# Kernel tuning notes

Hardware: AMD Instinct MI355X
Metric: run time of the kernel (lower is better)

Reference implementation:

```python
import jax, jax.numpy as jnp
import numpy as np

B, T, D_IN, D_H, D_CODE, N_CODES, D_OUT = 64, 512, 1024, 512, 256, 128, 100


def setup_inputs() -> dict:
    key = jax.random.key(0)
    ks = jax.random.split(key, 8)
    x = jax.random.normal(ks[0], (B, T, D_IN), dtype=jnp.float32)
    W1 = jax.random.normal(ks[1], (D_IN, D_H), dtype=jnp.float32) * (1.0 / np.sqrt(D_IN))
    b1 = jnp.zeros((D_H,), jnp.float32)
    W2 = jax.random.normal(ks[2], (D_H, D_CODE), dtype=jnp.float32) * (1.0 / np.sqrt(D_H))
    b2 = jnp.zeros((D_CODE,), jnp.float32)
    codebook = jax.random.normal(ks[3], (N_CODES, D_CODE), dtype=jnp.float32)
    Wd = jax.random.normal(ks[4], (D_CODE, D_OUT), dtype=jnp.float32) * (1.0 / np.sqrt(D_CODE))
    bd = jnp.zeros((D_OUT,), jnp.float32)
    return {"x": x, "W1": W1, "b1": b1, "W2": W2, "b2": b2,
            "codebook": codebook, "Wd": Wd, "bd": bd}


def reference(x, W1, b1, W2, b2, codebook, Wd, bd):
    Bb, Tt, _ = x.shape
    # Encoder (per-timestep loop in torch == one batched matmul)
    h = jax.nn.relu(jnp.einsum('btd,dh->bth', x, W1) + b1)
    encoded = jnp.einsum('bth,hc->btc', h, W2) + b2          # [B,T,256]
    flat = encoded.reshape(-1, D_CODE)                        # [B*T,256]
    # Squared euclidean distances (argmin identical to cdist argmin)
    d2 = (jnp.sum(flat * flat, axis=1, keepdims=True)
          - 2.0 * flat @ codebook.T
          + jnp.sum(codebook * codebook, axis=1))             # [B*T,128]
    token_indices = jnp.argmin(d2, axis=-1)                   # [B*T]
    quantized = codebook[token_indices].reshape(Bb, Tt, D_CODE)
    commitment_loss = jnp.mean((encoded - jax.lax.stop_gradient(quantized)) ** 2)
    codebook_loss = jnp.mean((quantized - jax.lax.stop_gradient(encoded)) ** 2)
    # decoded is computed in the torch model but never returned (dead code)
    pooled = encoded.mean(axis=1)
    decoded = pooled @ Wd + bd  # noqa: F841 (pruned by XLA, kept for fidelity)
    total_loss = commitment_loss + 0.25 * codebook_loss
    return (token_indices.reshape(Bb, Tt), commitment_loss, codebook_loss, total_loss)
```

## Files before the change

### kernel.cpp

```cpp
#include <hip/hip_runtime.h>
#include <cstddef>
#include <cstdint>

static constexpr int M_ROWS  = 32768;
static constexpr int D_INK   = 1024;
static constexpr int D_HID   = 512;
static constexpr int D_CODE_ = 256;
static constexpr int N_CODES_= 128;

static constexpr float TAU_GAP = 0.15f;

using f16x8 = __attribute__((ext_vector_type(8))) _Float16;
using f32x4 = __attribute__((ext_vector_type(4))) float;

__device__ __forceinline__ float rdlane(float v, int kk) {
    return __uint_as_float(__builtin_amdgcn_readlane(__float_as_uint(v), kk));
}


__device__ __forceinline__ void dma16(const void* g, void* l) {
    __builtin_amdgcn_global_load_lds(
        (const __attribute__((address_space(1))) void*)g,
        (__attribute__((address_space(3))) void*)l, 16, 0, 0);
}

__device__ __forceinline__ void stage_panel(const _Float16* __restrict__ p,
                                            _Float16* dst, int w, int lane)
{
    #pragma unroll
    for (int ii = 0; ii < 2; ++ii) {
        const int I = 2 * w + ii;
        dma16(p + (size_t)I * 512 + lane * 8, dst + (size_t)I * 512);
    }
}

__device__ __forceinline__ void mfma_tile(const _Float16* sA, const _Float16* sB,
                                          int wm, int wn, int kq, int lm,
                                          f32x4 (&acc)[4][4])
{
    f16x8 a[4];
    #pragma unroll
    for (int fm = 0; fm < 4; ++fm)
        a[fm] = *(const f16x8*)(sA + (kq * 128 + wm * 64 + fm * 16 + lm) * 8);
    #pragma unroll
    for (int fn = 0; fn < 4; ++fn) {
        const f16x8 b = *(const f16x8*)(sB + (kq * 128 + wn * 64 + fn * 16 + lm) * 8);
        #pragma unroll
        for (int fm = 0; fm < 4; ++fm)
            acc[fm][fn] = __builtin_amdgcn_mfma_f32_16x16x32_f16(a[fm], b, acc[fm][fn], 0, 0, 0);
    }
}

__device__ __forceinline__ int xcd_swz(int bid, int nwg) {
    const int q = nwg >> 3;
    return (bid & 7) * q + (bid >> 3);
}

__global__ __launch_bounds__(256)
void prep_cb_kernel(const float* __restrict__ cb, _Float16* __restrict__ cbP,
                    float* __restrict__ cbT,
                    float* __restrict__ cbnorm, float* __restrict__ accum,
                    int* __restrict__ cnt)
{
    const int j = blockIdx.x;
    const int t = threadIdx.x;
    const float v = cb[j * D_CODE_ + t];
    const int ks = t >> 5, kq = (t >> 3) & 3, jj = t & 7;
    cbP[((size_t)ks * 512 + kq * 128 + j) * 8 + jj] = (_Float16)v;
    cbT[(size_t)t * N_CODES_ + j] = v;

    __shared__ float sr[256];
    sr[t] = v * v;
    __syncthreads();
    for (int s = 128; s >= 1; s >>= 1) {
        if (t < s) sr[t] += sr[t + s];
        __syncthreads();
    }
    if (t == 0) cbnorm[j] = sr[0];
    if (j == 0 && t < 2) accum[t] = 0.0f;
    if (j == 0 && t == 2) *cnt = 0;
}

__global__ __launch_bounds__(256)
void pack_w_kernel(const float* __restrict__ W, _Float16* __restrict__ WP,
                   int Kd, int Nd)
{
    const int ks = blockIdx.x, nt = blockIdx.y;
    const int t = threadIdx.x;
    _Float16* dst = WP + ((size_t)nt * (Kd >> 5) + ks) * 4096;
    #pragma unroll
    for (int half = 0; half < 2; ++half) {
        const int f = half * 256 + t;
        const int nc = f & 127, kq = f >> 7;
        f16x8 v;
        #pragma unroll
        for (int j = 0; j < 8; ++j)
            v[j] = (_Float16)W[(size_t)(ks * 32 + kq * 8 + j) * Nd + nt * 128 + nc];
        *(f16x8*)(dst + (size_t)f * 8) = v;
    }
}

__global__ __launch_bounds__(256)
void pack_x_kernel(const float* __restrict__ X, _Float16* __restrict__ XP)
{
    __shared__ _Float16 sh[128][136];
    const int t  = threadIdx.x;
    const int mt = blockIdx.x;
    const int kc = blockIdx.y;

    const float* src = X + (size_t)mt * 128 * D_INK + kc * 128;
    #pragma unroll
    for (int i = 0; i < 16; ++i) {
        const int idx = i * 256 + t;
        const int row = idx >> 5, c4 = idx & 31;
        const float4 v = *(const float4*)(src + (size_t)row * D_INK + c4 * 4);
        _Float16* d = &sh[row][c4 * 4];
        d[0] = (_Float16)v.x; d[1] = (_Float16)v.y;
        d[2] = (_Float16)v.z; d[3] = (_Float16)v.w;
    }
    __syncthreads();

    _Float16* dst = XP + ((size_t)mt * 32 + kc * 4) * 4096;
    #pragma unroll
    for (int s = 0; s < 4; ++s) {
        #pragma unroll
        for (int half = 0; half < 2; ++half) {
            const int f = half * 256 + t;
            const int rc = f & 127, kq = f >> 7;
            const f16x8 v = *(const f16x8*)(&sh[rc][s * 32 + kq * 8]);
            *(f16x8*)(dst + (size_t)s * 4096 + (size_t)f * 8) = v;
        }
    }
}

__global__ __launch_bounds__(256, 4)
void gemm1_kernel(const _Float16* __restrict__ AP, const _Float16* __restrict__ BP,
                  const float* __restrict__ bias, _Float16* __restrict__ CP)
{
    __shared__ _Float16 lds[2][2][4096];

    const int tid  = threadIdx.x;
    const int lane = tid & 63;
    const int w    = tid >> 6;
    const int wm = w >> 1, wn = w & 1;
    const int kq = lane >> 4, lm = lane & 15;

    const int swz = xcd_swz(blockIdx.x, (M_ROWS / 128) * (D_HID / 128));
    const int n0 = (swz & 3) * 128;
    const int m0 = (swz >> 2) * 128;

    const _Float16* Apan = AP + ((size_t)(m0 >> 7) * 32) * 4096;
    const _Float16* Bpan = BP + ((size_t)(n0 >> 7) * 32) * 4096;

    f32x4 acc[4][4] = {};

    stage_panel(Apan, &lds[0][0][0], w, lane);
    stage_panel(Bpan, &lds[0][1][0], w, lane);

    constexpr int NSTEP = D_INK / 32;
    for (int t = 0; t < NSTEP; ++t) {
        const int cur = t & 1, nxt = cur ^ 1;
        __syncthreads();
        if (t + 1 < NSTEP) {
            stage_panel(Apan + (size_t)(t + 1) * 4096, &lds[nxt][0][0], w, lane);
            stage_panel(Bpan + (size_t)(t + 1) * 4096, &lds[nxt][1][0], w, lane);
        }
        mfma_tile(&lds[cur][0][0], &lds[cur][1][0], wm, wn, kq, lm, acc);
    }

    #pragma unroll
    for (int fn = 0; fn < 4; ++fn) {
        const int col = n0 + wn * 64 + fn * 16 + lm;
        const float bv = bias[col];
        #pragma unroll
        for (int fm = 0; fm < 4; ++fm) {
            #pragma unroll
            for (int r = 0; r < 4; ++r) {
                const int row = m0 + wm * 64 + fm * 16 + kq * 4 + r;
                const float v = fmaxf(acc[fm][fn][r] + bv, 0.0f);
                CP[(((size_t)(row >> 7) * 16 + (col >> 5)) * 512
                    + (size_t)((col >> 3) & 3) * 128 + (row & 127)) * 8 + (col & 7)]
                    = (_Float16)v;
            }
        }
    }
}

__global__ __launch_bounds__(256, 4)
void gemm2_kernel(const _Float16* __restrict__ AP, const _Float16* __restrict__ BP,
                  const float* __restrict__ bias, _Float16* __restrict__ CP,
                  float* __restrict__ accum)
{
    __shared__ _Float16 lds[2][2][4096];

    const int tid  = threadIdx.x;
    const int lane = tid & 63;
    const int w    = tid >> 6;
    const int wm = w >> 1, wn = w & 1;
    const int kq = lane >> 4, lm = lane & 15;

    const int swz = xcd_swz(blockIdx.x, (M_ROWS / 128) * (D_CODE_ / 128));
    const int n0 = (swz & 1) * 128;
    const int m0 = (swz >> 1) * 128;

    const _Float16* Apan = AP + ((size_t)(m0 >> 7) * 16) * 4096;
    const _Float16* Bpan = BP + ((size_t)(n0 >> 7) * 16) * 4096;

    f32x4 acc[4][4] = {};

    stage_panel(Apan, &lds[0][0][0], w, lane);
    stage_panel(Bpan, &lds[0][1][0], w, lane);

    constexpr int NSTEP = D_HID / 32;
    for (int t = 0; t < NSTEP; ++t) {
        const int cur = t & 1, nxt = cur ^ 1;
        __syncthreads();
        if (t + 1 < NSTEP) {
            stage_panel(Apan + (size_t)(t + 1) * 4096, &lds[nxt][0][0], w, lane);
            stage_panel(Bpan + (size_t)(t + 1) * 4096, &lds[nxt][1][0], w, lane);
        }
        mfma_tile(&lds[cur][0][0], &lds[cur][1][0], wm, wn, kq, lm, acc);
    }

    float sumsq = 0.0f;
    #pragma unroll
    for (int fn = 0; fn < 4; ++fn) {
        const int col = n0 + wn * 64 + fn * 16 + lm;
        const float bv = bias[col];
        #pragma unroll
        for (int fm = 0; fm < 4; ++fm) {
            #pragma unroll
            for (int r = 0; r < 4; ++r) {
                const int row = m0 + wm * 64 + fm * 16 + kq * 4 + r;
                const float v = acc[fm][fn][r] + bv;
                sumsq = fmaf(v, v, sumsq);
                CP[(((size_t)(row >> 7) * 8 + (col >> 5)) * 512
                    + (size_t)((col >> 3) & 3) * 128 + (row & 127)) * 8 + (col & 7)]
                    = (_Float16)v;
            }
        }
    }
    #pragma unroll
    for (int mk = 1; mk <= 32; mk <<= 1) sumsq += __shfl_xor(sumsq, mk);
    if (lane == 0) atomicAdd(&accum[1], sumsq);
}

__global__ __launch_bounds__(256, 4)
void dist_kernel(const _Float16* __restrict__ AP, const _Float16* __restrict__ BP,
                 const float* __restrict__ cbn,
                 float* __restrict__ outIdx, float* __restrict__ accum,
                 int* __restrict__ cnt, int* __restrict__ list)
{
    __shared__ _Float16 lds[2][2][4096];

    const int tid  = threadIdx.x;
    const int lane = tid & 63;
    const int w    = tid >> 6;
    const int wm = w >> 1, wn = w & 1;
    const int kq = lane >> 4, lm = lane & 15;
    const int m0 = blockIdx.x * 128;

    float cbn_l[4];
    #pragma unroll
    for (int fn = 0; fn < 4; ++fn) cbn_l[fn] = cbn[wn * 64 + fn * 16 + lm];

    const _Float16* Apan = AP + ((size_t)(m0 >> 7) * 8) * 4096;

    f32x4 acc[4][4] = {};

    stage_panel(Apan, &lds[0][0][0], w, lane);
    stage_panel(BP,   &lds[0][1][0], w, lane);

    constexpr int NSTEP = D_CODE_ / 32;
    for (int t = 0; t < NSTEP; ++t) {
        const int cur = t & 1, nxt = cur ^ 1;
        __syncthreads();
        if (t + 1 < NSTEP) {
            stage_panel(Apan + (size_t)(t + 1) * 4096, &lds[nxt][0][0], w, lane);
            stage_panel(BP   + (size_t)(t + 1) * 4096, &lds[nxt][1][0], w, lane);
        }
        mfma_tile(&lds[cur][0][0], &lds[cur][1][0], wm, wn, kq, lm, acc);
    }

    __syncthreads();
    float* eb1 = (float*)&lds[0][0][0];
    float* eb2 = eb1 + 256;
    int*   eix = (int*)(eb2 + 256);

    #pragma unroll
    for (int fm = 0; fm < 4; ++fm) {
        #pragma unroll
        for (int r = 0; r < 4; ++r) {
            float b1v = 3.4e38f, b2v = 3.4e38f; int bi = 0;
            #pragma unroll
            for (int fn = 0; fn < 4; ++fn) {
                const float v = fmaf(-2.0f, acc[fm][fn][r], cbn_l[fn]);
                if (v < b1v) { b2v = b1v; b1v = v; bi = wn * 64 + fn * 16 + lm; }
                else if (v < b2v) b2v = v;
            }
            #pragma unroll
            for (int mk = 1; mk <= 8; mk <<= 1) {
                const float o1 = __shfl_xor(b1v, mk);
                const float o2 = __shfl_xor(b2v, mk);
                const int   oi = __shfl_xor(bi,  mk);
                if (o1 < b1v || (o1 == b1v && oi < bi)) { b2v = fminf(b1v, o2); b1v = o1; bi = oi; }
                else b2v = fminf(b2v, o1);
            }
            const int rl = wm * 64 + fm * 16 + kq * 4 + r;
            if (lm == 0) { eb1[wn * 128 + rl] = b1v; eb2[wn * 128 + rl] = b2v; eix[wn * 128 + rl] = bi; }
        }
    }
    __syncthreads();

    if (tid < 128) {
        const int rl = tid;
        const float a1 = eb1[rl], a2 = eb2[rl]; const int ai = eix[rl];
        const float o1 = eb1[128 + rl], o2 = eb2[128 + rl]; const int oi = eix[128 + rl];
        float B1, B2; int BI;
        if (o1 < a1 || (o1 == a1 && oi < ai)) { B1 = o1; BI = oi; B2 = fminf(a1, o2); }
        else                                  { B1 = a1; BI = ai; B2 = fminf(a2, o1); }
        outIdx[m0 + rl] = (float)BI;
        if (B2 - B1 < TAU_GAP) { const int p = atomicAdd(cnt, 1); list[p] = m0 + rl; }
        float s = B1;
        #pragma unroll
        for (int mk = 1; mk <= 32; mk <<= 1) s += __shfl_xor(s, mk);
        if (lane == 0) atomicAdd(&accum[0], s);
    }
}

__global__ __launch_bounds__(512)
void fixup_kernel(const float* __restrict__ x, const float* __restrict__ W1,
                  const float* __restrict__ b1, const float* __restrict__ W2,
                  const float* __restrict__ b2, const float* __restrict__ cbT,
                  const float* __restrict__ cbnorm,
                  const int* __restrict__ cnt, const int* __restrict__ list,
                  float* __restrict__ outIdx)
{
    __shared__ float xr[8][1024];
    __shared__ float hr[8][512];
    __shared__ float er[8][256];
    __shared__ float dv[8][128];
    __shared__ int   di[8][128];

    const int tid  = threadIdx.x;
    const int lane = tid & 63;
    const int n = *cnt;
    const int ngroups = (n + 7) >> 3;

    for (int g = blockIdx.x; g < ngroups; g += gridDim.x) {
        const int base = g * 8;
        const int nr = n - base < 8 ? n - base : 8;
        __syncthreads();
        #pragma unroll
        for (int r = 0; r < 8; ++r) {
            if (r < nr) {
                const int row = list[base + r];
                *(float2*)&xr[r][tid * 2] =
                    *(const float2*)(x + (size_t)row * D_INK + tid * 2);
            }
        }
        __syncthreads();

        {
            const int c = tid;
            float a[8];
            #pragma unroll
            for (int r = 0; r < 8; ++r) a[r] = 0.f;
            for (int k0 = 0; k0 < D_INK; k0 += 64) {
                float xreg[8];
                #pragma unroll
                for (int r = 0; r < 8; ++r) xreg[r] = xr[r][k0 + lane];
                #pragma unroll 8
                for (int kk = 0; kk < 64; ++kk) {
                    const float wv = W1[(size_t)(k0 + kk) * D_HID + c];
                    #pragma unroll
                    for (int r = 0; r < 8; ++r)
                        a[r] = fmaf(rdlane(xreg[r], kk), wv, a[r]);
                }
            }
            #pragma unroll
            for (int r = 0; r < 8; ++r)
                hr[r][c] = fmaxf(a[r] + b1[c], 0.f);
        }
        __syncthreads();

        {
            const int c = tid & 255, half = tid >> 8;
            float a[4];
            #pragma unroll
            for (int q = 0; q < 4; ++q) a[q] = 0.f;
            for (int k0 = 0; k0 < D_HID; k0 += 64) {
                float hreg[4];
                #pragma unroll
                for (int q = 0; q < 4; ++q) hreg[q] = hr[half * 4 + q][k0 + lane];
                #pragma unroll 8
                for (int kk = 0; kk < 64; ++kk) {
                    const float wv = W2[(size_t)(k0 + kk) * D_CODE_ + c];
                    #pragma unroll
                    for (int q = 0; q < 4; ++q)
                        a[q] = fmaf(rdlane(hreg[q], kk), wv, a[q]);
                }
            }
            #pragma unroll
            for (int q = 0; q < 4; ++q)
                er[half * 4 + q][c] = a[q] + b2[c];
        }
        __syncthreads();

        {
            const int j = tid & 127, rr = tid >> 7;
            float e2[2], dt[2];
            #pragma unroll
            for (int q = 0; q < 2; ++q) { e2[q] = 0.f; dt[q] = 0.f; }
            for (int k0 = 0; k0 < D_CODE_; k0 += 64) {
                float ereg[2];
                ereg[0] = er[rr][k0 + lane];
                ereg[1] = er[rr + 4][k0 + lane];
                #pragma unroll 8
                for (int kk = 0; kk < 64; ++kk) {
                    const float cv = cbT[(size_t)(k0 + kk) * N_CODES_ + j];
                    #pragma unroll
                    for (int q = 0; q < 2; ++q) {
                        const float ev = rdlane(ereg[q], kk);
                        e2[q] = fmaf(ev, ev, e2[q]);
                        dt[q] = fmaf(ev, cv, dt[q]);
                    }
                }
            }
            dv[rr][j]     = (e2[0] - 2.0f * dt[0]) + cbnorm[j];
            di[rr][j]     = j;
            dv[rr + 4][j] = (e2[1] - 2.0f * dt[1]) + cbnorm[j];
            di[rr + 4][j] = j;
        }
        __syncthreads();

        #pragma unroll
        for (int pass = 0; pass < 2; ++pass) {
            const int r = pass * 4 + (tid >> 7);
            const int i = tid & 127;
            for (int st = 64; st >= 1; st >>= 1) {
                if (i < st) {
                    const float a = dv[r][i], b = dv[r][i + st];
                    const int  ib = di[r][i + st];
                    if (b < a || (b == a && ib < di[r][i])) { dv[r][i] = b; di[r][i] = ib; }
                }
                __syncthreads();
            }
        }
        if (tid < nr) outIdx[list[base + tid]] = (float)di[tid][0];
    }
}

__global__ void finalize_kernel(const float* __restrict__ accum, float* __restrict__ out)
{
    const float inv = 1.0f / (32768.0f * 256.0f);
    const float loss = (accum[0] + accum[1]) * inv;
    out[32768] = loss;
    out[32769] = loss;
    out[32770] = 1.25f * loss;
}

extern "C" void kernel_launch(void* const* d_in, const int* in_sizes, int n_in,
                              void* d_out, int out_size, void* d_ws, size_t ws_size,
                              hipStream_t stream)
{
    (void)in_sizes; (void)n_in; (void)out_size; (void)ws_size;

    const float* x  = (const float*)d_in[0];
    const float* W1 = (const float*)d_in[1];
    const float* b1 = (const float*)d_in[2];
    const float* W2 = (const float*)d_in[3];
    const float* b2 = (const float*)d_in[4];
    const float* cb = (const float*)d_in[5];
    float* out = (float*)d_out;

    char* ws = (char*)d_ws;
    _Float16* W1P  = (_Float16*)(ws + 0);
    _Float16* W2P  = (_Float16*)(ws + 1048576);
    _Float16* cbP  = (_Float16*)(ws + 1310720);
    float*    cbn  = (float*   )(ws + 1376256);
    float*    accum= (float*   )(ws + 1376768);
    int*      cnt  = (int*     )(ws + 1376832);
    int*      list = (int*     )(ws + 1376896);
    float*    cbT  = (float*   )(ws + 1507968);
    _Float16* xP   = (_Float16*)(ws + (size_t)(2u<<20));
    _Float16* encP = (_Float16*)(ws + (size_t)(2u<<20));
    _Float16* hP   = (_Float16*)(ws + (size_t)(2u<<20) + 67108864);

    prep_cb_kernel<<<N_CODES_, 256, 0, stream>>>(cb, cbP, cbT, cbn, accum, cnt);
    pack_w_kernel<<<dim3(D_INK / 32, D_HID / 128), 256, 0, stream>>>(W1, W1P, D_INK, D_HID);
    pack_w_kernel<<<dim3(D_HID / 32, D_CODE_ / 128), 256, 0, stream>>>(W2, W2P, D_HID, D_CODE_);
    pack_x_kernel<<<dim3(M_ROWS / 128, D_INK / 128), 256, 0, stream>>>(x, xP);

    gemm1_kernel<<<(M_ROWS / 128) * (D_HID / 128), 256, 0, stream>>>(xP, W1P, b1, hP);
    gemm2_kernel<<<(M_ROWS / 128) * (D_CODE_ / 128), 256, 0, stream>>>(hP, W2P, b2, encP, accum);
    dist_kernel<<<M_ROWS / 128, 256, 0, stream>>>(encP, cbP, cbn, out, accum, cnt, list);
    fixup_kernel<<<512, 512, 0, stream>>>(x, W1, b1, W2, b2, cbT, cbn, cnt, list, out);
    finalize_kernel<<<1, 1, 0, stream>>>(accum, out);
}
```

Baseline: 275.2 us.

## Restructure fixup kernel to one wavefront per row with shuffle argmin

The exact-recompute fixup kernel now assigns each of the 8 rows in a group to its own wavefront. Each lane computes 8, 4, then 2 output columns using vectorized weight loads and lane broadcasts. The block-wide __syncthreads barriers and the shared-memory tree argmin are replaced by a wave-level shuffle reduction. This is meant to remove barrier overhead and idle threads in the fallback path. In exchange, each wavefront now streams the full weight matrices on its own, so weight reuse across rows is lost.

```diff
diff --git a/kernel.cpp b/kernel.cpp
--- a/kernel.cpp
+++ b/kernel.cpp
@@ -339,115 +339,97 @@
     __shared__ float xr[8][1024];
     __shared__ float hr[8][512];
     __shared__ float er[8][256];
-    __shared__ float dv[8][128];
-    __shared__ int   di[8][128];
 
     const int tid  = threadIdx.x;
     const int lane = tid & 63;
+    const int wid  = tid >> 6;
     const int n = *cnt;
     const int ngroups = (n + 7) >> 3;
 
     for (int g = blockIdx.x; g < ngroups; g += gridDim.x) {
-        const int base = g * 8;
-        const int nr = n - base < 8 ? n - base : 8;
-        __syncthreads();
-        #pragma unroll
-        for (int r = 0; r < 8; ++r) {
-            if (r < nr) {
-                const int row = list[base + r];
-                *(float2*)&xr[r][tid * 2] =
-                    *(const float2*)(x + (size_t)row * D_INK + tid * 2);
-            }
-        }
-        __syncthreads();
-
+        const int ridx = g * 8 + wid;
+        if (ridx >= n) continue;
+        const int row = list[ridx];
+        const float* xrow = x + (size_t)row * D_INK;
+
+        #pragma unroll
+        for (int i = 0; i < 4; ++i)
+            *(float4*)&xr[wid][i * 256 + lane * 4] =
+                *(const float4*)(xrow + i * 256 + lane * 4);
+
+        const int c0 = lane * 8;
+        float4 a0 = {0.f, 0.f, 0.f, 0.f}, a1 = {0.f, 0.f, 0.f, 0.f};
+        for (int k0 = 0; k0 < D_INK; k0 += 64) {
+            const float xreg = xr[wid][k0 + lane];
+            #pragma unroll
+            for (int kk = 0; kk < 64; ++kk) {
+                const float* wrow = W1 + (size_t)(k0 + kk) * D_HID + c0;
+                const float4 w0 = *(const float4*)(wrow);
+                const float4 w1 = *(const float4*)(wrow + 4);
+                const float xb = rdlane(xreg, kk);
+                a0.x = fmaf(xb, w0.x, a0.x); a0.y = fmaf(xb, w0.y, a0.y);
+                a0.z = fmaf(xb, w0.z, a0.z); a0.w = fmaf(xb, w0.w, a0.w);
+                a1.x = fmaf(xb, w1.x, a1.x); a1.y = fmaf(xb, w1.y, a1.y);
+                a1.z = fmaf(xb, w1.z, a1.z); a1.w = fmaf(xb, w1.w, a1.w);
+            }
+        }
         {
-            const int c = tid;
-            float a[8];
-            #pragma unroll
-            for (int r = 0; r < 8; ++r) a[r] = 0.f;
-            for (int k0 = 0; k0 < D_INK; k0 += 64) {
-                float xreg[8];
-                #pragma unroll
-                for (int r = 0; r < 8; ++r) xreg[r] = xr[r][k0 + lane];
-                #pragma unroll 8
-                for (int kk = 0; kk < 64; ++kk) {
-                    const float wv = W1[(size_t)(k0 + kk) * D_HID + c];
-                    #pragma unroll
-                    for (int r = 0; r < 8; ++r)
-                        a[r] = fmaf(rdlane(xreg[r], kk), wv, a[r]);
-                }
-            }
-            #pragma unroll
-            for (int r = 0; r < 8; ++r)
-                hr[r][c] = fmaxf(a[r] + b1[c], 0.f);
-        }
-        __syncthreads();
-
+            const float4 bb0 = *(const float4*)(b1 + c0);
+            const float4 bb1 = *(const float4*)(b1 + c0 + 4);
+            float4 h0, h1;
+            h0.x = fmaxf(a0.x + bb0.x, 0.f); h0.y = fmaxf(a0.y + bb0.y, 0.f);
+            h0.z = fmaxf(a0.z + bb0.z, 0.f); h0.w = fmaxf(a0.w + bb0.w, 0.f);
+            h1.x = fmaxf(a1.x + bb1.x, 0.f); h1.y = fmaxf(a1.y + bb1.y, 0.f);
+            h1.z = fmaxf(a1.z + bb1.z, 0.f); h1.w = fmaxf(a1.w + bb1.w, 0.f);
+            *(float4*)&hr[wid][c0]     = h0;
+            *(float4*)&hr[wid][c0 + 4] = h1;
+        }
+
+        const int d0 = lane * 4;
+        float4 e4 = {0.f, 0.f, 0.f, 0.f};
+        for (int k0 = 0; k0 < D_HID; k0 += 64) {
+            const float hreg = hr[wid][k0 + lane];
+            #pragma unroll
+            for (int kk = 0; kk < 64; ++kk) {
+                const float4 wv = *(const float4*)(W2 + (size_t)(k0 + kk) * D_CODE_ + d0);
+                const float hb = rdlane(hreg, kk);
+                e4.x = fmaf(hb, wv.x, e4.x); e4.y = fmaf(hb, wv.y, e4.y);
+                e4.z = fmaf(hb, wv.z, e4.z); e4.w = fmaf(hb, wv.w, e4.w);
+            }
+        }
         {
-            const int c = tid & 255, half = tid >> 8;
-            float a[4];
-            #pragma unroll
-            for (int q = 0; q < 4; ++q) a[q] = 0.f;
-            for (int k0 = 0; k0 < D_HID; k0 += 64) {
-                float hreg[4];
-                #pragma unroll
-                for (int q = 0; q < 4; ++q) hreg[q] = hr[half * 4 + q][k0 + lane];
-                #pragma unroll 8
-                for (int kk = 0; kk < 64; ++kk) {
-                    const float wv = W2[(size_t)(k0 + kk) * D_CODE_ + c];
-                    #pragma unroll
-                    for (int q = 0; q < 4; ++q)
-                        a[q] = fmaf(rdlane(hreg[q], kk), wv, a[q]);
-                }
-            }
-            #pragma unroll
-            for (int q = 0; q < 4; ++q)
-                er[half * 4 + q][c] = a[q] + b2[c];
-        }
-        __syncthreads();
-
-        {
-            const int j = tid & 127, rr = tid >> 7;
-            float e2[2], dt[2];
-            #pragma unroll
-            for (int q = 0; q < 2; ++q) { e2[q] = 0.f; dt[q] = 0.f; }
-            for (int k0 = 0; k0 < D_CODE_; k0 += 64) {
-                float ereg[2];
-                ereg[0] = er[rr][k0 + lane];
-                ereg[1] = er[rr + 4][k0 + lane];
-                #pragma unroll 8
-                for (int kk = 0; kk < 64; ++kk) {
-                    const float cv = cbT[(size_t)(k0 + kk) * N_CODES_ + j];
-                    #pragma unroll
-                    for (int q = 0; q < 2; ++q) {
-                        const float ev = rdlane(ereg[q], kk);
-                        e2[q] = fmaf(ev, ev, e2[q]);
-                        dt[q] = fmaf(ev, cv, dt[q]);
-                    }
-                }
-            }
-            dv[rr][j]     = (e2[0] - 2.0f * dt[0]) + cbnorm[j];
-            di[rr][j]     = j;
-            dv[rr + 4][j] = (e2[1] - 2.0f * dt[1]) + cbnorm[j];
-            di[rr + 4][j] = j;
-        }
-        __syncthreads();
-
-        #pragma unroll
-        for (int pass = 0; pass < 2; ++pass) {
-            const int r = pass * 4 + (tid >> 7);
-            const int i = tid & 127;
-            for (int st = 64; st >= 1; st >>= 1) {
-                if (i < st) {
-                    const float a = dv[r][i], b = dv[r][i + st];
-                    const int  ib = di[r][i + st];
-                    if (b < a || (b == a && ib < di[r][i])) { dv[r][i] = b; di[r][i] = ib; }
-                }
-                __syncthreads();
-            }
-        }
-        if (tid < nr) outIdx[list[base + tid]] = (float)di[tid][0];
+            const float4 bb = *(const float4*)(b2 + d0);
+            float4 ev;
+            ev.x = e4.x + bb.x; ev.y = e4.y + bb.y;
+            ev.z = e4.z + bb.z; ev.w = e4.w + bb.w;
+            *(float4*)&er[wid][d0] = ev;
+        }
+
+        const int j0 = lane * 2;
+        float e2 = 0.f, dt0 = 0.f, dt1 = 0.f;
+        for (int k0 = 0; k0 < D_CODE_; k0 += 64) {
+            const float ereg = er[wid][k0 + lane];
+            #pragma unroll
+            for (int kk = 0; kk < 64; ++kk) {
+                const float2 cv = *(const float2*)(cbT + (size_t)(k0 + kk) * N_CODES_ + j0);
+                const float ev = rdlane(ereg, kk);
+                e2  = fmaf(ev, ev, e2);
+                dt0 = fmaf(ev, cv.x, dt0);
+                dt1 = fmaf(ev, cv.y, dt1);
+            }
+        }
+        const float dva = (e2 - 2.0f * dt0) + cbnorm[j0];
+        const float dvb = (e2 - 2.0f * dt1) + cbnorm[j0 + 1];
+        float bv; int bi;
+        if (dvb < dva) { bv = dvb; bi = j0 + 1; } else { bv = dva; bi = j0; }
+
+        #pragma unroll
+        for (int mk = 1; mk <= 32; mk <<= 1) {
+            const float ov = __shfl_xor(bv, mk);
+            const int   oi = __shfl_xor(bi, mk);
+            if (ov < bv || (ov == bv && oi < bi)) { bv = ov; bi = oi; }
+        }
+        if (lane == 0) outIdx[row] = (float)bi;
     }
 }
 
```

New measurement: 495.0 us. 1.8x slower.
